# Kernel tuning notes

Hardware: AMD Instinct MI355X
Metric: run time of the kernel (lower is better)

## Reference

```python
import jax, jax.numpy as jnp
import numpy as np

N = 50000   # nodes per graph
E = 800000  # edges per graph (even, message() splits in half)
F = 100     # node/edge feature dim (init_count_size / init_emb_size)
D = 64      # hidden_dim3 = rule_graph_dim
W_SCALE = 0.05


def _mlp(x, w1, b1, w2, b2):
    return jax.nn.relu(x @ w1 + b1) @ w2 + b2


def _triple_conv(x, src, dst, ea, lw, lb, l2w, l2b, nn_fn):
    # PyG flow source_to_target: x_j = x[edge_index[0]], x_i = x[edge_index[1]]
    h = ea.shape[0] // 2
    x_j = x[src]
    x_i = x[dst]
    m1 = jax.nn.relu(jnp.concatenate([x_i[:h], ea[:h], x_j[:h]], 1) @ lw + lb)
    m2 = jax.nn.relu(jnp.concatenate([x_j[h:], ea[h:], x_i[h:]], 1) @ l2w + l2b)
    msgs = jnp.concatenate([m1, m2], 0)
    agg = jax.ops.segment_sum(msgs, dst, num_segments=x.shape[0])
    # eps = 0.0 buffer -> out = agg + (1+eps)*x = agg + x
    return nn_fn(agg + x)


def setup_inputs() -> dict:
    key = jax.random.key(0)
    ks = jax.random.split(key, 32)
    inp = {
        'features_1': jax.random.normal(ks[0], (N, F), jnp.float32),
        'edge_index_1': jax.random.randint(ks[1], (2, E), 0, N, jnp.int64 if jax.config.jax_enable_x64 else jnp.int32).astype(jnp.int32),
        'edge_attr_1': jax.random.normal(ks[2], (E, F), jnp.float32),
        'features_2': jax.random.normal(ks[3], (N, F), jnp.float32),
        'edge_index_2': jax.random.randint(ks[4], (2, E), 0, N, jnp.int32),
        'edge_attr_2': jax.random.normal(ks[5], (E, F), jnp.float32),
        'c1_lin_w': jax.random.normal(ks[6], (3 * F, F), jnp.float32) * W_SCALE,
        'c1_lin_b': jax.random.normal(ks[7], (F,), jnp.float32) * W_SCALE,
        'c1_lin2_w': jax.random.normal(ks[8], (3 * F, F), jnp.float32) * W_SCALE,
        'c1_lin2_b': jax.random.normal(ks[9], (F,), jnp.float32) * W_SCALE,
        'mlp1_w1': jax.random.normal(ks[10], (F, F), jnp.float32) * W_SCALE,
        'mlp1_b1': jax.random.normal(ks[11], (F,), jnp.float32) * W_SCALE,
        'mlp1_w2': jax.random.normal(ks[12], (F, F), jnp.float32) * W_SCALE,
        'mlp1_b2': jax.random.normal(ks[13], (F,), jnp.float32) * W_SCALE,
        'c2_lin_w': jax.random.normal(ks[14], (3 * F, F), jnp.float32) * W_SCALE,
        'c2_lin_b': jax.random.normal(ks[15], (F,), jnp.float32) * W_SCALE,
        'c2_lin2_w': jax.random.normal(ks[16], (3 * F, F), jnp.float32) * W_SCALE,
        'c2_lin2_b': jax.random.normal(ks[17], (F,), jnp.float32) * W_SCALE,
        'mlp2_w1': jax.random.normal(ks[18], (F, D), jnp.float32) * W_SCALE,
        'mlp2_b1': jax.random.normal(ks[19], (D,), jnp.float32) * W_SCALE,
        'mlp2_w2': jax.random.normal(ks[20], (D, D), jnp.float32) * W_SCALE,
        'mlp2_b2': jax.random.normal(ks[21], (D,), jnp.float32) * W_SCALE,
    }
    return inp


def reference(features_1, edge_index_1, edge_attr_1,
              features_2, edge_index_2, edge_attr_2,
              c1_lin_w, c1_lin_b, c1_lin2_w, c1_lin2_b,
              mlp1_w1, mlp1_b1, mlp1_w2, mlp1_b2,
              c2_lin_w, c2_lin_b, c2_lin2_w, c2_lin2_b,
              mlp2_w1, mlp2_b1, mlp2_w2, mlp2_b2):

    def conv_pass(x, ei, ea):
        src, dst = ei[0], ei[1]
        x = _triple_conv(x, src, dst, ea, c1_lin_w, c1_lin_b, c1_lin2_w, c1_lin2_b,
                         lambda z: _mlp(z, mlp1_w1, mlp1_b1, mlp1_w2, mlp1_b2))
        x = jax.nn.relu(x)
        x = _triple_conv(x, src, dst, ea, c2_lin_w, c2_lin_b, c2_lin2_w, c2_lin2_b,
                         lambda z: _mlp(z, mlp2_w1, mlp2_b1, mlp2_w2, mlp2_b2))
        return x

    f1 = conv_pass(features_1, edge_index_1, edge_attr_1)  # [N, D]
    f2 = conv_pass(features_2, edge_index_2, edge_attr_2)  # [N, D]
    # global_add_pool with a single batch id -> sum over nodes
    g1 = jnp.sum(f1, axis=0)
    g2 = jnp.sum(f2, axis=0)
    return jnp.stack([g1, g2], 0)  # [2, D]
```

## Files before the change

### kernel.cpp

```cpp
#include <hip/hip_runtime.h>

#define F 100
#define TS 256

typedef __attribute__((ext_vector_type(4))) unsigned short us4;
typedef __attribute__((ext_vector_type(8))) short short8;
typedef __attribute__((ext_vector_type(4))) float f32x4;

static __device__ __forceinline__ unsigned short f2bf(float f) {
    unsigned int u = __float_as_uint(f);
    unsigned int r = (u + 0x7FFF + ((u >> 16) & 1)) >> 16;
    return (unsigned short)r;
}
static __device__ __forceinline__ float bf2f(unsigned short u) {
    return __uint_as_float(((unsigned int)u) << 16);
}
static __device__ __forceinline__ short8 cvt8(float4 v0, float4 v1) {
    short8 a;
    a[0] = (short)f2bf(v0.x); a[1] = (short)f2bf(v0.y);
    a[2] = (short)f2bf(v0.z); a[3] = (short)f2bf(v0.w);
    a[4] = (short)f2bf(v1.x); a[5] = (short)f2bf(v1.y);
    a[6] = (short)f2bf(v1.z); a[7] = (short)f2bf(v1.w);
    return a;
}

__global__ __launch_bounds__(TS)
void hist2_kernel(const int* __restrict__ dst0, const int* __restrict__ dst1,
                  int h, int E, int N,
                  int* __restrict__ cnt1, int* __restrict__ cnt2)
{
    for (int idx = blockIdx.x * TS + threadIdx.x; idx < 2 * E; idx += gridDim.x * TS) {
        int g = idx >= E;
        int e = idx - g * E;
        int d = (g ? dst1 : dst0)[e];
        atomicAdd((e < h ? cnt1 : cnt2) + g * N + d, 1);
    }
}

__global__ __launch_bounds__(1024)
void scan4_kernel(const int* __restrict__ cnt1, const int* __restrict__ cnt2,
                  int* __restrict__ rp1, int* __restrict__ rp2, int n)
{
    const int which = blockIdx.x;
    const int hf = which >> 1, g = which & 1;
    const int* cnt = (hf ? cnt2 : cnt1) + g * n;
    int* rp = (hf ? rp2 : rp1) + g * (n + 1);
    __shared__ int buf[1024];
    __shared__ int carry_s;
    const int t = threadIdx.x;
    if (t == 0) carry_s = 0;
    __syncthreads();
    for (int base = 0; base < n; base += 8192) {
        int v[8], s = 0;
        #pragma unroll
        for (int j = 0; j < 8; ++j) {
            int idx = base + t * 8 + j;
            int x = (idx < n) ? cnt[idx] : 0;
            v[j] = s; s += x;
        }
        buf[t] = s;
        __syncthreads();
        for (int off = 1; off < 1024; off <<= 1) {
            int y = (t >= off) ? buf[t - off] : 0;
            __syncthreads();
            buf[t] += y;
            __syncthreads();
        }
        int excl = carry_s + buf[t] - s;
        #pragma unroll
        for (int j = 0; j < 8; ++j) {
            int idx = base + t * 8 + j;
            if (idx < n) rp[idx] = excl + v[j];
        }
        __syncthreads();
        if (t == 1023) carry_s += buf[1023];
        __syncthreads();
    }
    if (t == 0) rp[n] = carry_s;
}

__global__ __launch_bounds__(TS)
void scatter2_kernel(const int* __restrict__ src0, const int* __restrict__ dst0,
                     const int* __restrict__ src1, const int* __restrict__ dst1,
                     int h, int E, int N,
                     const int* __restrict__ rp1, const int* __restrict__ rp2,
                     int* __restrict__ cur1, int* __restrict__ cur2,
                     int* __restrict__ perm1, int* __restrict__ perm2,
                     int* __restrict__ es1, int* __restrict__ es2)
{
    for (int idx = blockIdx.x * TS + threadIdx.x; idx < 2 * E; idx += gridDim.x * TS) {
        int g = idx >= E;
        int e = idx - g * E;
        int d = (g ? dst1 : dst0)[e];
        int s = (g ? src1 : src0)[e];
        if (e < h) {
            int p = rp1[g * (N + 1) + d] + atomicAdd(&cur1[g * N + d], 1);
            perm1[g * h + p] = e; es1[g * h + p] = s + g * N;
        } else {
            int p = rp2[g * (N + 1) + d] + atomicAdd(&cur2[g * N + d], 1);
            perm2[g * h + p] = e; es2[g * h + p] = s + g * N;
        }
    }
}

__global__ __launch_bounds__(TS)
void pack_w_kernel(const float* w0, const float* w1, const float* w2, const float* w3,
                   unsigned short* __restrict__ Wp)
{
    int i = blockIdx.x * TS + threadIdx.x;
    if (i >= 12 * 112 * 128) return;
    int s = i / (112 * 128);
    int r = i - s * (112 * 128);
    int c = r >> 7, k = r & 127;
    int wi = s & 3, grp = s >> 2;
    const float* w = (wi == 0) ? w0 : (wi == 1) ? w1 : (wi == 2) ? w2 : w3;
    int off = (grp == 0) ? F : ((grp == 1) ? 0 : 2 * F);
    unsigned short v = 0;
    if (c < 100 && k < 100) v = f2bf(w[(off + k) * F + c]);
    Wp[i] = v;
}

__global__ __launch_bounds__(TS)
void pack_w2_kernel(const float* __restrict__ w, int K, int Nc, int ldb,
                    unsigned short* __restrict__ out)
{
    int i = blockIdx.x * TS + threadIdx.x;
    if (i >= 112 * 128) return;
    int c = i >> 7, k = i & 127;
    unsigned short v = 0;
    if (c < Nc && k < K) v = f2bf(w[k * ldb + c]);
    out[i] = v;
}

__global__ __launch_bounds__(TS)
void pack_x2_kernel(const float* __restrict__ x0, const float* __restrict__ x1,
                    int N, unsigned short* __restrict__ xb)
{
    const size_t total = (size_t)N * 2 * 32;
    for (size_t i = (size_t)blockIdx.x * TS + threadIdx.x; i < total; i += (size_t)gridDim.x * TS) {
        int n = (int)(i >> 5), q = (int)(i & 31);
        int g = n >= N;
        const float* x = g ? x1 : x0;
        int nl = n - g * N;
        us4 o = (us4){0, 0, 0, 0};
        if (q < 25) {
            float4 v = *(const float4*)&x[(size_t)nl * 100 + q * 4];
            o.x = f2bf(v.x); o.y = f2bf(v.y); o.z = f2bf(v.z); o.w = f2bf(v.w);
        }
        *(us4*)&xb[((size_t)n << 7) + q * 4] = o;
    }
}

__global__ __launch_bounds__(TS)
void pack_sum2_f32(const float* __restrict__ agg,
                   const float* __restrict__ x0, const float* __restrict__ x1,
                   int N, unsigned short* __restrict__ Ab)
{
    const size_t total = (size_t)N * 2 * 32;
    for (size_t i = (size_t)blockIdx.x * TS + threadIdx.x; i < total; i += (size_t)gridDim.x * TS) {
        int n = (int)(i >> 5), q = (int)(i & 31);
        int g = n >= N;
        const float* x = g ? x1 : x0;
        int nl = n - g * N;
        us4 o = (us4){0, 0, 0, 0};
        if (q < 25) {
            float4 a = *(const float4*)&agg[(size_t)n * 100 + q * 4];
            float4 v = *(const float4*)&x[(size_t)nl * 100 + q * 4];
            o.x = f2bf(a.x + v.x); o.y = f2bf(a.y + v.y);
            o.z = f2bf(a.z + v.z); o.w = f2bf(a.w + v.w);
        }
        *(us4*)&Ab[((size_t)n << 7) + q * 4] = o;
    }
}

__global__ __launch_bounds__(TS)
void pack_sum_bf16(const float* __restrict__ agg, const unsigned short* __restrict__ xb,
                   int M, unsigned short* __restrict__ Ab)
{
    const size_t total = (size_t)M * 32;
    for (size_t i = (size_t)blockIdx.x * TS + threadIdx.x; i < total; i += (size_t)gridDim.x * TS) {
        int n = (int)(i >> 5), q = (int)(i & 31);
        us4 o = (us4){0, 0, 0, 0};
        if (q < 25) {
            float4 a = *(const float4*)&agg[(size_t)n * 100 + q * 4];
            us4 v = *(const us4*)&xb[((size_t)n << 7) + q * 4];
            o.x = f2bf(a.x + bf2f(v.x)); o.y = f2bf(a.y + bf2f(v.y));
            o.z = f2bf(a.z + bf2f(v.z)); o.w = f2bf(a.w + bf2f(v.w));
        }
        *(us4*)&Ab[((size_t)n << 7) + q * 4] = o;
    }
}

__global__ __launch_bounds__(TS)
void gemm_node_mfma(const unsigned short* __restrict__ xb,
                    const unsigned short* __restrict__ B0, const unsigned short* __restrict__ B1,
                    const unsigned short* __restrict__ B2, const unsigned short* __restrict__ B3,
                    unsigned short* __restrict__ NTb,
                    int M)
{
    const int t = threadIdx.x, lane = t & 63, wv = t >> 6;
    const int rA = lane & 15, kg = lane >> 4;
    const unsigned short* Bp[4] = {B0, B1, B2, B3};
    const int ntiles = (M + 15) >> 4;
    for (int tile = blockIdx.x * 4 + wv; tile < ntiles; tile += gridDim.x * 4) {
        const int base = tile << 4;
        const int arow = min(base + rA, M - 1);
        short8 A[4];
        #pragma unroll
        for (int ks = 0; ks < 4; ++ks)
            A[ks] = *(const short8*)&xb[((size_t)arow << 7) + ks * 32 + kg * 8];
        const int row = base + rA;
        #pragma unroll
        for (int sel = 0; sel < 4; ++sel) {
            const unsigned short* B = Bp[sel];
            f32x4 C[7];
            #pragma unroll
            for (int nf = 0; nf < 7; ++nf) C[nf] = (f32x4){0.f, 0.f, 0.f, 0.f};
            #pragma unroll
            for (int ks = 0; ks < 4; ++ks) {
                #pragma unroll
                for (int nf = 0; nf < 7; ++nf) {
                    short8 Bf = *(const short8*)&B[(size_t)(rA + nf * 16) * 128 + ks * 32 + kg * 8];
                    C[nf] = __builtin_amdgcn_mfma_f32_16x16x32_bf16(Bf, A[ks], C[nf], 0, 0, 0);
                }
            }
            if (row < M) {
                #pragma unroll
                for (int nf = 0; nf < 7; ++nf) {
                    const int cb = nf * 16 + kg * 4;
                    if (cb < 100) {
                        us4 o;
                        o.x = f2bf(C[nf][0]); o.y = f2bf(C[nf][1]);
                        o.z = f2bf(C[nf][2]); o.w = f2bf(C[nf][3]);
                        *(us4*)&NTb[(size_t)row * 400 + sel * 100 + cb] = o;
                    }
                }
            }
        }
    }
}

static __device__ __forceinline__ void gather_ea(const float* __restrict__ ea0,
                                                 const float* __restrict__ ea1,
                                                 const int* __restrict__ perm,
                                                 int row, int h, int kg, short8* A)
{
    const int g = row >= h;
    const int e = perm[row];
    const float* ea = (g ? ea1 : ea0) + (size_t)e * 100;
    #pragma unroll
    for (int ks = 0; ks < 3; ++ks) {
        float4 v0 = *(const float4*)&ea[ks * 32 + kg * 8];
        float4 v1 = *(const float4*)&ea[ks * 32 + kg * 8 + 4];
        A[ks] = cvt8(v0, v1);
    }
    short8 a3 = (short8){0, 0, 0, 0, 0, 0, 0, 0};
    if (kg == 0) {
        float4 v = *(const float4*)&ea[96];
        a3[0] = (short)f2bf(v.x); a3[1] = (short)f2bf(v.y);
        a3[2] = (short)f2bf(v.z); a3[3] = (short)f2bf(v.w);
    }
    A[3] = a3;
}

__global__ __launch_bounds__(TS)
void gemm_edge_quad(const float* __restrict__ ea0, const float* __restrict__ ea1,
                    const int* __restrict__ perm,
                    const unsigned short* __restrict__ W0,
                    const unsigned short* __restrict__ W1,
                    unsigned short* __restrict__ P0,
                    unsigned short* __restrict__ P1,
                    int h)
{
    const int t = threadIdx.x, lane = t & 63, wv = t >> 6;
    const int rA = lane & 15, kg = lane >> 4;
    const int M = 2 * h;
    const int ntiles = M >> 4;
    const int stride = gridDim.x * 4;
    int tile = blockIdx.x * 4 + wv;
    if (tile >= ntiles) return;

    short8 Acur[4], Anxt[4];
    gather_ea(ea0, ea1, perm, (tile << 4) + rA, h, kg, Acur);

    while (true) {
        const int tn = tile + stride;
        const bool more = tn < ntiles;
        if (more) gather_ea(ea0, ea1, perm, (tn << 4) + rA, h, kg, Anxt);

        f32x4 C0[7], C1[7];
        #pragma unroll
        for (int nf = 0; nf < 7; ++nf) {
            C0[nf] = (f32x4){0.f, 0.f, 0.f, 0.f};
            C1[nf] = (f32x4){0.f, 0.f, 0.f, 0.f};
        }
        #pragma unroll
        for (int ks = 0; ks < 4; ++ks) {
            #pragma unroll
            for (int nf = 0; nf < 7; ++nf) {
                short8 B0f = *(const short8*)&W0[(size_t)(rA + nf * 16) * 128 + ks * 32 + kg * 8];
                C0[nf] = __builtin_amdgcn_mfma_f32_16x16x32_bf16(B0f, Acur[ks], C0[nf], 0, 0, 0);
                short8 B1f = *(const short8*)&W1[(size_t)(rA + nf * 16) * 128 + ks * 32 + kg * 8];
                C1[nf] = __builtin_amdgcn_mfma_f32_16x16x32_bf16(B1f, Acur[ks], C1[nf], 0, 0, 0);
            }
        }
        const int row = (tile << 4) + rA;
        #pragma unroll
        for (int nf = 0; nf < 7; ++nf) {
            const int cb = nf * 16 + kg * 4;
            if (cb < 100) {
                us4 o0, o1;
                o0.x = f2bf(C0[nf][0]); o0.y = f2bf(C0[nf][1]);
                o0.z = f2bf(C0[nf][2]); o0.w = f2bf(C0[nf][3]);
                o1.x = f2bf(C1[nf][0]); o1.y = f2bf(C1[nf][1]);
                o1.z = f2bf(C1[nf][2]); o1.w = f2bf(C1[nf][3]);
                *(us4*)&P0[(size_t)row * 100 + cb] = o0;
                *(us4*)&P1[(size_t)row * 100 + cb] = o1;
            }
        }
        if (!more) break;
        #pragma unroll
        for (int i = 0; i < 4; ++i) Acur[i] = Anxt[i];
        tile = tn;
    }
}

__global__ __launch_bounds__(TS)
void seg_reduce_both(const unsigned short* __restrict__ PA,
                     const unsigned short* __restrict__ PB,
                     const int* __restrict__ es1, const int* __restrict__ es2,
                     const int* __restrict__ rp1, const int* __restrict__ rp2,
                     const float* __restrict__ cb, const float* __restrict__ cb2,
                     const unsigned short* __restrict__ NTb,
                     float* __restrict__ agg,
                     int N, int h)
{
    const int gid = blockIdx.x * TS + threadIdx.x;
    const int n = gid >> 5, q = gid & 31;
    if (n >= 2 * N || q >= 25) return;
    const int c4 = q * 4;
    const int g = n >= N;
    const int nl = n - g * N;

    float ax = 0.f, ay = 0.f, az = 0.f, aw = 0.f;

    {
        const us4 vd = *(const us4*)&NTb[(size_t)n * 400 + 0 * 100 + c4];
        const float4 bi = *(const float4*)&cb[c4];
        const float dx = bf2f(vd.x) + bi.x, dy = bf2f(vd.y) + bi.y;
        const float dz = bf2f(vd.z) + bi.z, dw = bf2f(vd.w) + bi.w;
        const int* rpg = rp1 + g * (N + 1);
        int p0 = max(rpg[nl], 0) + g * h;
        int p1 = min(rpg[nl + 1], h) + g * h;
        for (int pos = p0; pos < p1; ++pos) {
            const int s = es1[pos];
            const us4 pv = *(const us4*)&PA[(size_t)pos * 100 + c4];
            const us4 vs = *(const us4*)&NTb[(size_t)s * 400 + 1 * 100 + c4];
            ax += fmaxf(bf2f(pv.x) + bf2f(vs.x) + dx, 0.f);
            ay += fmaxf(bf2f(pv.y) + bf2f(vs.y) + dy, 0.f);
            az += fmaxf(bf2f(pv.z) + bf2f(vs.z) + dz, 0.f);
            aw += fmaxf(bf2f(pv.w) + bf2f(vs.w) + dw, 0.f);
        }
    }
    {
        const us4 vd = *(const us4*)&NTb[(size_t)n * 400 + 3 * 100 + c4];
        const float4 bi = *(const float4*)&cb2[c4];
        const float dx = bf2f(vd.x) + bi.x, dy = bf2f(vd.y) + bi.y;
        const float dz = bf2f(vd.z) + bi.z, dw = bf2f(vd.w) + bi.w;
        const int* rpg = rp2 + g * (N + 1);
        int p0 = max(rpg[nl], 0) + g * h;
        int p1 = min(rpg[nl + 1], h) + g * h;
        for (int pos = p0; pos < p1; ++pos) {
            const int s = es2[pos];
            const us4 pv = *(const us4*)&PB[(size_t)pos * 100 + c4];
            const us4 vs = *(const us4*)&NTb[(size_t)s * 400 + 2 * 100 + c4];
            ax += fmaxf(bf2f(pv.x) + bf2f(vs.x) + dx, 0.f);
            ay += fmaxf(bf2f(pv.y) + bf2f(vs.y) + dy, 0.f);
            az += fmaxf(bf2f(pv.z) + bf2f(vs.z) + dz, 0.f);
            aw += fmaxf(bf2f(pv.w) + bf2f(vs.w) + dw, 0.f);
        }
    }
    float* ap = &agg[(size_t)n * 100 + c4];
    ap[0] = ax; ap[1] = ay; ap[2] = az; ap[3] = aw;
}

__global__ __launch_bounds__(TS)
void gemm_mlp_bf16out(const unsigned short* __restrict__ Ab,
                      const unsigned short* __restrict__ Wp,
                      const float* __restrict__ bias,
                      unsigned short* __restrict__ out,
                      int M, int Nc)
{
    const int t = threadIdx.x, lane = t & 63, wv = t >> 6;
    const int rA = lane & 15, kg = lane >> 4;
    const int ntiles = (M + 15) >> 4;
    for (int tile = blockIdx.x * 4 + wv; tile < ntiles; tile += gridDim.x * 4) {
        const int base = tile << 4;
        const int arow = min(base + rA, M - 1);
        f32x4 C[7];
        #pragma unroll
        for (int nf = 0; nf < 7; ++nf) C[nf] = (f32x4){0.f, 0.f, 0.f, 0.f};
        #pragma unroll
        for (int ks = 0; ks < 4; ++ks) {
            short8 A = *(const short8*)&Ab[((size_t)arow << 7) + ks * 32 + kg * 8];
            #pragma unroll
            for (int nf = 0; nf < 7; ++nf) {
                short8 B = *(const short8*)&Wp[(size_t)(rA + nf * 16) * 128 + ks * 32 + kg * 8];
                C[nf] = __builtin_amdgcn_mfma_f32_16x16x32_bf16(B, A, C[nf], 0, 0, 0);
            }
        }
        const int row = base + rA;
        if (row < M) {
            #pragma unroll
            for (int nf = 0; nf < 7; ++nf) {
                const int cb = nf * 16 + kg * 4;
                us4 o = (us4){0, 0, 0, 0};
                if (cb < Nc) {
                    float4 bv = *(const float4*)&bias[cb];
                    o.x = f2bf(fmaxf(C[nf][0] + bv.x, 0.f));
                    o.y = f2bf(fmaxf(C[nf][1] + bv.y, 0.f));
                    o.z = f2bf(fmaxf(C[nf][2] + bv.z, 0.f));
                    o.w = f2bf(fmaxf(C[nf][3] + bv.w, 0.f));
                }
                *(us4*)&out[((size_t)row << 7) + cb] = o;
            }
            *(us4*)&out[((size_t)row << 7) + 112 + kg * 4] = (us4){0, 0, 0, 0};
        }
    }
}

__global__ __launch_bounds__(TS)
void gemm_mlp_f32out(const unsigned short* __restrict__ Ab,
                     const unsigned short* __restrict__ Wp,
                     const float* __restrict__ bias,
                     float* __restrict__ out,
                     int M)
{
    const int t = threadIdx.x, lane = t & 63, wv = t >> 6;
    const int rA = lane & 15, kg = lane >> 4;
    const int ntiles = (M + 15) >> 4;
    for (int tile = blockIdx.x * 4 + wv; tile < ntiles; tile += gridDim.x * 4) {
        const int base = tile << 4;
        const int arow = min(base + rA, M - 1);
        f32x4 C[4];
        #pragma unroll
        for (int nf = 0; nf < 4; ++nf) C[nf] = (f32x4){0.f, 0.f, 0.f, 0.f};
        #pragma unroll
        for (int ks = 0; ks < 2; ++ks) {
            short8 A = *(const short8*)&Ab[((size_t)arow << 7) + ks * 32 + kg * 8];
            #pragma unroll
            for (int nf = 0; nf < 4; ++nf) {
                short8 B = *(const short8*)&Wp[(size_t)(rA + nf * 16) * 128 + ks * 32 + kg * 8];
                C[nf] = __builtin_amdgcn_mfma_f32_16x16x32_bf16(B, A, C[nf], 0, 0, 0);
            }
        }
        const int row = base + rA;
        if (row < M) {
            #pragma unroll
            for (int nf = 0; nf < 4; ++nf) {
                const int cb = nf * 16 + kg * 4;
                float4 bv = *(const float4*)&bias[cb];
                float4 o;
                o.x = C[nf][0] + bv.x; o.y = C[nf][1] + bv.y;
                o.z = C[nf][2] + bv.z; o.w = C[nf][3] + bv.w;
                *(float4*)&out[(size_t)row * 64 + cb] = o;
            }
        }
    }
}

__global__ __launch_bounds__(TS)
void colsum2_kernel(const float* __restrict__ Fm, int N, float* __restrict__ out)
{
    __shared__ float red[4][2][64];
    const int t = threadIdx.x;
    const int c = t & 63, rg = t >> 6;
    float s0 = 0.f, s1 = 0.f;
    const int M = 2 * N;
    for (int r = blockIdx.x * 4 + rg; r < M; r += gridDim.x * 4) {
        float v = Fm[(size_t)r * 64 + c];
        if (r < N) s0 += v; else s1 += v;
    }
    red[rg][0][c] = s0; red[rg][1][c] = s1;
    __syncthreads();
    if (rg == 0) {
        atomicAdd(&out[c],      red[0][0][c] + red[1][0][c] + red[2][0][c] + red[3][0][c]);
        atomicAdd(&out[64 + c], red[0][1][c] + red[1][1][c] + red[2][1][c] + red[3][1][c]);
    }
}

extern "C" void kernel_launch(void* const* d_in, const int* in_sizes, int n_in,
                              void* d_out, int out_size, void* d_ws, size_t ws_size,
                              hipStream_t stream)
{
    const int N = in_sizes[0] / F;
    const int E = in_sizes[1] / 2;
    const int h = E / 2;
    const int N2 = 2 * N, h2 = 2 * h;

    unsigned short* NTb  = (unsigned short*)d_ws;
    float* AGG = (float*)(NTb + (size_t)N2 * 400);
    unsigned short* P1A = (unsigned short*)(AGG + (size_t)N2 * 100);
    unsigned short* P1B = P1A + (size_t)h2 * 100;
    unsigned short* P2A = P1B + (size_t)h2 * 100;
    unsigned short* P2B = P2A + (size_t)h2 * 100;
    unsigned short* xb  = P2B + (size_t)h2 * 100;
    unsigned short* X1b = xb + (size_t)N2 * 128;
    unsigned short* Ab  = X1b + (size_t)N2 * 128;
    unsigned short* Hb  = Ab + (size_t)N2 * 128;
    int* rp1   = (int*)(Hb + (size_t)N2 * 128);
    int* rp2   = rp1 + 2 * (N + 1);
    int* cnt1  = rp2 + 2 * (N + 1);
    int* cnt2  = cnt1 + N2;
    int* perm1 = cnt2 + N2;
    int* perm2 = perm1 + h2;
    int* es1   = perm2 + h2;
    int* es2   = es1 + h2;
    unsigned short* Wp = (unsigned short*)(es2 + h2);
    unsigned short* Wm = Wp + (size_t)12 * 112 * 128;
    float* F2 = AGG;

    const float* x0g0 = (const float*)d_in[0];
    const int*   ei0  = (const int*)d_in[1];
    const float* ea0  = (const float*)d_in[2];
    const float* x0g1 = (const float*)d_in[3];
    const int*   ei1  = (const int*)d_in[4];
    const float* ea1  = (const float*)d_in[5];
    const float* c1w  = (const float*)d_in[6];
    const float* c1b  = (const float*)d_in[7];
    const float* c1w2 = (const float*)d_in[8];
    const float* c1b2 = (const float*)d_in[9];
    const float* m1w1 = (const float*)d_in[10];
    const float* m1b1 = (const float*)d_in[11];
    const float* m1w2 = (const float*)d_in[12];
    const float* m1b2 = (const float*)d_in[13];
    const float* c2w  = (const float*)d_in[14];
    const float* c2b  = (const float*)d_in[15];
    const float* c2w2 = (const float*)d_in[16];
    const float* c2b2 = (const float*)d_in[17];
    const float* m2w1 = (const float*)d_in[18];
    const float* m2b1 = (const float*)d_in[19];
    const float* m2w2 = (const float*)d_in[20];
    const float* m2b2 = (const float*)d_in[21];

    hipMemsetAsync(d_out, 0, (size_t)out_size * sizeof(float), stream);

    const dim3 blk(TS);
    const size_t SL = (size_t)112 * 128;
    pack_w_kernel<<<(12 * 112 * 128 + TS - 1) / TS, blk, 0, stream>>>(c1w, c1w2, c2w, c2w2, Wp);
    pack_w2_kernel<<<56, blk, 0, stream>>>(m1w1, 100, 100, 100, Wm + 0 * SL);
    pack_w2_kernel<<<56, blk, 0, stream>>>(m1w2, 100, 100, 100, Wm + 1 * SL);
    pack_w2_kernel<<<56, blk, 0, stream>>>(m2w1, 100,  64,  64, Wm + 2 * SL);
    pack_w2_kernel<<<56, blk, 0, stream>>>(m2w2,  64,  64,  64, Wm + 3 * SL);

    hipMemsetAsync(cnt1, 0, 2 * (size_t)N2 * sizeof(int), stream);
    hist2_kernel<<<2048, blk, 0, stream>>>(ei0 + E, ei1 + E, h, E, N, cnt1, cnt2);
    scan4_kernel<<<4, 1024, 0, stream>>>(cnt1, cnt2, rp1, rp2, N);
    hipMemsetAsync(cnt1, 0, 2 * (size_t)N2 * sizeof(int), stream);
    scatter2_kernel<<<2048, blk, 0, stream>>>(ei0, ei0 + E, ei1, ei1 + E, h, E, N,
                                              rp1, rp2, cnt1, cnt2, perm1, perm2, es1, es2);
    pack_x2_kernel<<<2048, blk, 0, stream>>>(x0g0, x0g1, N, xb);

    gemm_edge_quad<<<4096, blk, 0, stream>>>(ea0, ea1, perm1,
                                             Wp + 0 * SL, Wp + 2 * SL, P1A, P2A, h);
    gemm_edge_quad<<<4096, blk, 0, stream>>>(ea0, ea1, perm2,
                                             Wp + 1 * SL, Wp + 3 * SL, P1B, P2B, h);

    const int nblkR = (N2 * 32 + TS - 1) / TS;
    for (int conv = 0; conv < 2; ++conv) {
        const float* cb  = conv ? c2b  : c1b;
        const float* cb2 = conv ? c2b2 : c1b2;
        const unsigned short* xin = conv ? X1b : xb;
        const int iw  = conv ? 2 : 0;
        const int iw2 = conv ? 3 : 1;
        const unsigned short* PA = conv ? P2A : P1A;
        const unsigned short* PB = conv ? P2B : P1B;

        gemm_node_mfma<<<2048, blk, 0, stream>>>(xin,
            Wp + (size_t)(4 + iw)  * SL, Wp + (size_t)(8 + iw)  * SL,
            Wp + (size_t)(4 + iw2) * SL, Wp + (size_t)(8 + iw2) * SL,
            NTb, N2);

        seg_reduce_both<<<nblkR, blk, 0, stream>>>(PA, PB, es1, es2, rp1, rp2,
                                                   cb, cb2, NTb, AGG, N, h);

        if (conv == 0) {
            pack_sum2_f32<<<2048, blk, 0, stream>>>(AGG, x0g0, x0g1, N, Ab);
            gemm_mlp_bf16out<<<2048, blk, 0, stream>>>(Ab, Wm + 0 * SL, m1b1, Hb,  N2, 100);
            gemm_mlp_bf16out<<<2048, blk, 0, stream>>>(Hb, Wm + 1 * SL, m1b2, X1b, N2, 100);
        } else {
            pack_sum_bf16<<<2048, blk, 0, stream>>>(AGG, X1b, N2, Ab);
            gemm_mlp_bf16out<<<2048, blk, 0, stream>>>(Ab, Wm + 2 * SL, m2b1, Hb, N2, 64);
            gemm_mlp_f32out<<<2048, blk, 0, stream>>>(Hb, Wm + 3 * SL, m2b2, F2, N2);
        }
    }
    colsum2_kernel<<<512, blk, 0, stream>>>(F2, N, (float*)d_out);
    (void)ws_size; (void)n_in;
}
```

Measured before the change: 1.568 ms.

## Stage gathered edge attributes through double-buffered LDS with coalesced row loads

The edge GEMM now gathers each 64-row group cooperatively. Four threads load one edge row as contiguous float4s, convert it to bf16 and write it into a double-buffered shared tile, and the MFMA operands are then read from LDS. This replaces the per-lane strided fragment gathers and is meant to improve coalescing of the random-row reads, prefetching the next group while the current one is computed. It adds LDS use, block-wide barriers and half the grid size, which may reduce latency hiding.

Result: faster. 1.463 ms (-6.7%).

```diff
diff --git a/kernel.cpp b/kernel.cpp
--- a/kernel.cpp
+++ b/kernel.cpp
@@ -14,14 +14,6 @@
 }
 static __device__ __forceinline__ float bf2f(unsigned short u) {
     return __uint_as_float(((unsigned int)u) << 16);
-}
-static __device__ __forceinline__ short8 cvt8(float4 v0, float4 v1) {
-    short8 a;
-    a[0] = (short)f2bf(v0.x); a[1] = (short)f2bf(v0.y);
-    a[2] = (short)f2bf(v0.z); a[3] = (short)f2bf(v0.w);
-    a[4] = (short)f2bf(v1.x); a[5] = (short)f2bf(v1.y);
-    a[6] = (short)f2bf(v1.z); a[7] = (short)f2bf(v1.w);
-    return a;
 }
 
 __global__ __launch_bounds__(TS)
@@ -240,29 +232,6 @@
     }
 }
 
-static __device__ __forceinline__ void gather_ea(const float* __restrict__ ea0,
-                                                 const float* __restrict__ ea1,
-                                                 const int* __restrict__ perm,
-                                                 int row, int h, int kg, short8* A)
-{
-    const int g = row >= h;
-    const int e = perm[row];
-    const float* ea = (g ? ea1 : ea0) + (size_t)e * 100;
-    #pragma unroll
-    for (int ks = 0; ks < 3; ++ks) {
-        float4 v0 = *(const float4*)&ea[ks * 32 + kg * 8];
-        float4 v1 = *(const float4*)&ea[ks * 32 + kg * 8 + 4];
-        A[ks] = cvt8(v0, v1);
-    }
-    short8 a3 = (short8){0, 0, 0, 0, 0, 0, 0, 0};
-    if (kg == 0) {
-        float4 v = *(const float4*)&ea[96];
-        a3[0] = (short)f2bf(v.x); a3[1] = (short)f2bf(v.y);
-        a3[2] = (short)f2bf(v.z); a3[3] = (short)f2bf(v.w);
-    }
-    A[3] = a3;
-}
-
 __global__ __launch_bounds__(TS)
 void gemm_edge_quad(const float* __restrict__ ea0, const float* __restrict__ ea1,
                     const int* __restrict__ perm,
@@ -272,56 +241,111 @@
                     unsigned short* __restrict__ P1,
                     int h)
 {
+    __shared__ unsigned short sA[2][64][136];
     const int t = threadIdx.x, lane = t & 63, wv = t >> 6;
     const int rA = lane & 15, kg = lane >> 4;
     const int M = 2 * h;
-    const int ntiles = M >> 4;
-    const int stride = gridDim.x * 4;
-    int tile = blockIdx.x * 4 + wv;
-    if (tile >= ntiles) return;
-
-    short8 Acur[4], Anxt[4];
-    gather_ea(ea0, ea1, perm, (tile << 4) + rA, h, kg, Acur);
-
+    const int ngrp = M >> 6;
+    const int r_loc = t >> 2, sub = t & 3;
+
+    int grp = blockIdx.x;
+    if (grp >= ngrp) return;
+
+    {
+        const int grow = (grp << 6) + r_loc;
+        const int g = grow >= h;
+        const int e = perm[grow];
+        const float* ea = (g ? ea1 : ea0) + (size_t)e * 100;
+        float4 raw[7];
+        #pragma unroll
+        for (int j = 0; j < 7; ++j) {
+            const int q = sub + 4 * j;
+            if (q < 25) raw[j] = *(const float4*)&ea[q * 4];
+        }
+        #pragma unroll
+        for (int j = 0; j < 8; ++j) {
+            const int q = sub + 4 * j;
+            us4 o = (us4){0, 0, 0, 0};
+            if (j < 7 && q < 25) {
+                o.x = f2bf(raw[j].x); o.y = f2bf(raw[j].y);
+                o.z = f2bf(raw[j].z); o.w = f2bf(raw[j].w);
+            }
+            if (q < 32) *(us4*)&sA[0][r_loc][q * 4] = o;
+        }
+    }
+    __syncthreads();
+
+    int cur = 0;
     while (true) {
-        const int tn = tile + stride;
-        const bool more = tn < ntiles;
-        if (more) gather_ea(ea0, ea1, perm, (tn << 4) + rA, h, kg, Anxt);
-
-        f32x4 C0[7], C1[7];
-        #pragma unroll
-        for (int nf = 0; nf < 7; ++nf) {
-            C0[nf] = (f32x4){0.f, 0.f, 0.f, 0.f};
-            C1[nf] = (f32x4){0.f, 0.f, 0.f, 0.f};
-        }
-        #pragma unroll
-        for (int ks = 0; ks < 4; ++ks) {
+        const int nxt = grp + gridDim.x;
+        const bool more = nxt < ngrp;
+
+        float4 raw[7];
+        if (more) {
+            const int grow = (nxt << 6) + r_loc;
+            const int g = grow >= h;
+            const int e = perm[grow];
+            const float* ea = (g ? ea1 : ea0) + (size_t)e * 100;
+            #pragma unroll
+            for (int j = 0; j < 7; ++j) {
+                const int q = sub + 4 * j;
+                if (q < 25) raw[j] = *(const float4*)&ea[q * 4];
+            }
+        }
+
+        {
+            const int lrow = wv * 16 + rA;
+            short8 A[4];
+            #pragma unroll
+            for (int ks = 0; ks < 4; ++ks)
+                A[ks] = *(const short8*)&sA[cur][lrow][ks * 32 + kg * 8];
+
+            f32x4 C0[7], C1[7];
             #pragma unroll
             for (int nf = 0; nf < 7; ++nf) {
-                short8 B0f = *(const short8*)&W0[(size_t)(rA + nf * 16) * 128 + ks * 32 + kg * 8];
-                C0[nf] = __builtin_amdgcn_mfma_f32_16x16x32_bf16(B0f, Acur[ks], C0[nf], 0, 0, 0);
-                short8 B1f = *(const short8*)&W1[(size_t)(rA + nf * 16) * 128 + ks * 32 + kg * 8];
-                C1[nf] = __builtin_amdgcn_mfma_f32_16x16x32_bf16(B1f, Acur[ks], C1[nf], 0, 0, 0);
-            }
-        }
-        const int row = (tile << 4) + rA;
-        #pragma unroll
-        for (int nf = 0; nf < 7; ++nf) {
-            const int cb = nf * 16 + kg * 4;
-            if (cb < 100) {
-                us4 o0, o1;
-                o0.x = f2bf(C0[nf][0]); o0.y = f2bf(C0[nf][1]);
-                o0.z = f2bf(C0[nf][2]); o0.w = f2bf(C0[nf][3]);
-                o1.x = f2bf(C1[nf][0]); o1.y = f2bf(C1[nf][1]);
-                o1.z = f2bf(C1[nf][2]); o1.w = f2bf(C1[nf][3]);
-                *(us4*)&P0[(size_t)row * 100 + cb] = o0;
-                *(us4*)&P1[(size_t)row * 100 + cb] = o1;
-            }
-        }
+                C0[nf] = (f32x4){0.f, 0.f, 0.f, 0.f};
+                C1[nf] = (f32x4){0.f, 0.f, 0.f, 0.f};
+            }
+            #pragma unroll
+            for (int ks = 0; ks < 4; ++ks) {
+                #pragma unroll
+                for (int nf = 0; nf < 7; ++nf) {
+                    short8 B0f = *(const short8*)&W0[(size_t)(rA + nf * 16) * 128 + ks * 32 + kg * 8];
+                    C0[nf] = __builtin_amdgcn_mfma_f32_16x16x32_bf16(B0f, A[ks], C0[nf], 0, 0, 0);
+                    short8 B1f = *(const short8*)&W1[(size_t)(rA + nf * 16) * 128 + ks * 32 + kg * 8];
+                    C1[nf] = __builtin_amdgcn_mfma_f32_16x16x32_bf16(B1f, A[ks], C1[nf], 0, 0, 0);
+                }
+            }
+            const int row = (grp << 6) + lrow;
+            #pragma unroll
+            for (int nf = 0; nf < 7; ++nf) {
+                const int cb = nf * 16 + kg * 4;
+                if (cb < 100) {
+                    us4 o0, o1;
+                    o0.x = f2bf(C0[nf][0]); o0.y = f2bf(C0[nf][1]);
+                    o0.z = f2bf(C0[nf][2]); o0.w = f2bf(C0[nf][3]);
+                    o1.x = f2bf(C1[nf][0]); o1.y = f2bf(C1[nf][1]);
+                    o1.z = f2bf(C1[nf][2]); o1.w = f2bf(C1[nf][3]);
+                    *(us4*)&P0[(size_t)row * 100 + cb] = o0;
+                    *(us4*)&P1[(size_t)row * 100 + cb] = o1;
+                }
+            }
+        }
+
         if (!more) break;
-        #pragma unroll
-        for (int i = 0; i < 4; ++i) Acur[i] = Anxt[i];
-        tile = tn;
+
+        #pragma unroll
+        for (int j = 0; j < 8; ++j) {
+            const int q = sub + 4 * j;
+            us4 o = (us4){0, 0, 0, 0};
+            if (j < 7 && q < 25) {
+                o.x = f2bf(raw[j].x); o.y = f2bf(raw[j].y);
+                o.z = f2bf(raw[j].z); o.w = f2bf(raw[j].w);
+            }
+            if (q < 32) *(us4*)&sA[cur ^ 1][r_loc][q * 4] = o;
+        }
+        __syncthreads();
+        cur ^= 1; grp = nxt;
     }
 }
 
@@ -561,9 +585,9 @@
                                               rp1, rp2, cnt1, cnt2, perm1, perm2, es1, es2);
     pack_x2_kernel<<<2048, blk, 0, stream>>>(x0g0, x0g1, N, xb);
 
-    gemm_edge_quad<<<4096, blk, 0, stream>>>(ea0, ea1, perm1,
+    gemm_edge_quad<<<2048, blk, 0, stream>>>(ea0, ea1, perm1,
                                              Wp + 0 * SL, Wp + 2 * SL, P1A, P2A, h);
-    gemm_edge_quad<<<4096, blk, 0, stream>>>(ea0, ea1, perm2,
+    gemm_edge_quad<<<2048, blk, 0, stream>>>(ea0, ea1, perm2,
                                              Wp + 1 * SL, Wp + 3 * SL, P1B, P2B, h);
 
     const int nblkR = (N2 * 32 + TS - 1) / TS;
```
